# Performance work log

Hardware: AMD Instinct MI355X
Metric: run time of the kernel (lower is better)

The kernel has to match this reference:

```python
import jax, jax.numpy as jnp
import jax.scipy.linalg as jsl
import numpy as np

EPS = 1e-6          # config.eps
MIN_EIG = 1e-4      # config.min_eigenvalue
B, N, K = 2, 2048, 3


def _so3_generators():
    # standard so(3) basis: [G_c]_{kl} = -eps_{ckl}
    G = np.zeros((3, 3, 3), np.float32)
    G[0, 1, 2] = -1.0; G[0, 2, 1] = 1.0
    G[1, 0, 2] = 1.0;  G[1, 2, 0] = -1.0
    G[2, 0, 1] = -1.0; G[2, 1, 0] = 1.0
    return jnp.asarray(G)


def _spd(key, b, n, k):
    # well-conditioned SPD covariances (as a real model would produce)
    A = jax.random.normal(key, (b, n, k, k), jnp.float32)
    return jnp.einsum('bnkl,bnml->bnkm', A, A) / k + 0.5 * jnp.eye(k, dtype=jnp.float32)


def setup_inputs() -> dict:
    key = jax.random.key(0)
    k0, k1, k2, k3 = jax.random.split(key, 4)
    Sigma_prior = _spd(k0, B, N, K)
    Sigma_q = _spd(k1, B, N, K)
    phi = jax.random.normal(k2, (B, N, K), jnp.float32)          # gauge field, C == K == 3
    beta = jax.random.uniform(k3, (B, N, N), jnp.float32) / N    # attention-like weights, rows O(1)
    return {
        'Sigma_prior': Sigma_prior,
        'Sigma_q': Sigma_q,
        'phi': phi,
        'beta': beta,
        'generators': _so3_generators(),
    }


def _batched_expm(mats):
    # mats: (B, N, K, K) -> elementwise matrix exponential
    b, n, k, _ = mats.shape
    return jax.vmap(jsl.expm)(mats.reshape(-1, k, k)).reshape(b, n, k, k)


def reference(Sigma_prior, Sigma_q, phi, beta, generators):
    b, n, k, _ = Sigma_prior.shape
    I = jnp.eye(k, dtype=Sigma_prior.dtype)

    # precisions (regularized inverses)
    Lambda_p = jnp.linalg.inv(Sigma_prior + EPS * I)   # (B,N,K,K)
    Lambda_q = jnp.linalg.inv(Sigma_q + EPS * I)       # (B,N,K,K)

    # gauge transport Omega_ij = e^{phi_i} e^{-phi_j}
    phi_mat = jnp.einsum('bnc,ckl->bnkl', phi, generators)
    exp_phi = _batched_expm(phi_mat)
    exp_neg_phi = _batched_expm(-phi_mat)
    Omega = jnp.einsum('bikl,bjlm->bijkm', exp_phi, exp_neg_phi)   # (B,N,N,K,K)

    # transported neighbor precision: Omega Lambda_q Omega^T
    Lt = jnp.einsum('bijkl,bjlm,bijnm->bijkn', Omega, Lambda_q, Omega)

    # incoming social term: sum_j beta_ij * Lt_ij
    M_in = jnp.einsum('bij,bijkl->bikl', beta, Lt)

    # outgoing recoil: (sum_j beta_ji) * Lambda_q_i
    M_out = beta.sum(axis=1)[..., None, None] * Lambda_q

    M = Lambda_p + M_in + M_out
    M = 0.5 * (M + jnp.swapaxes(M, -1, -2))

    # eigenvalue floor + inverse via eigh
    w, V = jnp.linalg.eigh(M)
    w = jnp.maximum(w, MIN_EIG)
    M_pd = jnp.einsum('bnkl,bnl,bnml->bnkm', V, w, V)
    M_inv = jnp.einsum('bnkl,bnl,bnml->bnkm', V, 1.0 / w, V)
    return M_pd, M_inv
```

## Files before the change

kernel.cpp:

```cpp
#include <hip/hip_runtime.h>
#include <math.h>

#define EPS_REG 1e-6f
#define MIN_EIG_F 1e-4f
#define RB 8


__device__ __forceinline__ void sym_inv3(const float m[3][3], float o[3][3]) {
    float c00 = m[1][1]*m[2][2] - m[1][2]*m[2][1];
    float c01 = m[1][2]*m[2][0] - m[1][0]*m[2][2];
    float c02 = m[1][0]*m[2][1] - m[1][1]*m[2][0];
    float det = m[0][0]*c00 + m[0][1]*c01 + m[0][2]*c02;
    float inv = 1.0f / det;
    o[0][0] = c00*inv;
    o[1][0] = c01*inv;
    o[2][0] = c02*inv;
    o[0][1] = (m[0][2]*m[2][1]-m[0][1]*m[2][2])*inv;
    o[1][1] = (m[0][0]*m[2][2]-m[0][2]*m[2][0])*inv;
    o[2][1] = (m[0][1]*m[2][0]-m[0][0]*m[2][1])*inv;
    o[0][2] = (m[0][1]*m[1][2]-m[0][2]*m[1][1])*inv;
    o[1][2] = (m[0][2]*m[1][0]-m[0][0]*m[1][2])*inv;
    o[2][2] = (m[0][0]*m[1][1]-m[0][1]*m[1][0])*inv;
}

__device__ __forceinline__ void rodrigues(float w0, float w1, float w2, float R[3][3]) {
    float th2 = w0*w0 + w1*w1 + w2*w2;
    float th = sqrtf(th2);
    float a, b;
    if (th < 1e-4f) { a = 1.0f - th2*(1.0f/6.0f); b = 0.5f - th2*(1.0f/24.0f); }
    else            { a = sinf(th)/th;            b = (1.0f - cosf(th))/th2; }
    R[0][0] = 1.0f + b*(w0*w0 - th2); R[0][1] = -a*w2 + b*w0*w1;        R[0][2] =  a*w1 + b*w0*w2;
    R[1][0] =  a*w2 + b*w0*w1;        R[1][1] = 1.0f + b*(w1*w1 - th2); R[1][2] = -a*w0 + b*w1*w2;
    R[2][0] = -a*w1 + b*w0*w2;        R[2][1] =  a*w0 + b*w1*w2;        R[2][2] = 1.0f + b*(w2*w2 - th2);
}

__device__ __forceinline__ void jrot(float A[3][3], float V[3][3], int p, int q) {
    float apq = A[p][q];
    if (fabsf(apq) < 1e-20f) return;
    float theta = (A[q][q] - A[p][p]) / (2.0f * apq);
    float t = 1.0f / (fabsf(theta) + sqrtf(1.0f + theta*theta));
    if (theta < 0.0f) t = -t;
    float c = 1.0f / sqrtf(1.0f + t*t);
    float s = t * c;
    int r = 3 - p - q;
    float apq_t = t*apq;
    A[p][p] -= apq_t;
    A[q][q] += apq_t;
    A[p][q] = 0.0f; A[q][p] = 0.0f;
    float arp = A[r][p], arq = A[r][q];
    A[r][p] = c*arp - s*arq; A[p][r] = A[r][p];
    A[r][q] = s*arp + c*arq; A[q][r] = A[r][q];
    #pragma unroll
    for (int k = 0; k < 3; k++) {
        float vkp = V[k][p], vkq = V[k][q];
        V[k][p] = c*vkp - s*vkq;
        V[k][q] = s*vkp + c*vkq;
    }
}

__global__ __launch_bounds__(64) void precompute_S_kernel(
        const float* __restrict__ Sq,
        const float* __restrict__ phi,
        float* __restrict__ Splanes,
        int BN) {
    __shared__ float sq_s[576];
    __shared__ float ph_s[192];
    int tid = threadIdx.x;
    int p0 = blockIdx.x * 64;

    const float4* src = (const float4*)(Sq + (size_t)p0 * 9);
    #pragma unroll
    for (int i = tid; i < 144; i += 64) ((float4*)sq_s)[i] = src[i];
    const float4* psrc = (const float4*)(phi + (size_t)p0 * 3);
    if (tid < 48) ((float4*)ph_s)[tid] = psrc[tid];
    __syncthreads();

    float m[3][3], lq[3][3];
    #pragma unroll
    for (int i = 0; i < 3; i++)
        #pragma unroll
        for (int j = 0; j < 3; j++) m[i][j] = sq_s[tid*9 + i*3 + j];
    m[0][0] += EPS_REG; m[1][1] += EPS_REG; m[2][2] += EPS_REG;
    sym_inv3(m, lq);

    float R[3][3];
    rodrigues(ph_s[tid*3], ph_s[tid*3+1], ph_s[tid*3+2], R);

    float U[3][3];
    #pragma unroll
    for (int i = 0; i < 3; i++)
        #pragma unroll
        for (int j = 0; j < 3; j++)
            U[i][j] = lq[i][0]*R[0][j] + lq[i][1]*R[1][j] + lq[i][2]*R[2][j];
    float sv[6];
    sv[0] = R[0][0]*U[0][0] + R[1][0]*U[1][0] + R[2][0]*U[2][0];
    sv[1] = R[0][0]*U[0][1] + R[1][0]*U[1][1] + R[2][0]*U[2][1];
    sv[2] = R[0][0]*U[0][2] + R[1][0]*U[1][2] + R[2][0]*U[2][2];
    sv[3] = R[0][1]*U[0][1] + R[1][1]*U[1][1] + R[2][1]*U[2][1];
    sv[4] = R[0][1]*U[0][2] + R[1][1]*U[1][2] + R[2][1]*U[2][2];
    sv[5] = R[0][2]*U[0][2] + R[1][2]*U[1][2] + R[2][2]*U[2][2];
    #pragma unroll
    for (int c = 0; c < 6; c++)
        Splanes[(size_t)c * BN + p0 + tid] = sv[c];
}

__global__ __launch_bounds__(256) void fused_beta_kernel(
        const float* __restrict__ beta,
        const float* __restrict__ Splanes,
        float* __restrict__ T,
        float* __restrict__ partial,
        int B, int N, int BN) {
    int tid = threadIdx.x;
    int grow0 = blockIdx.x * RB;
    int b = grow0 / N;
    int chunksPerB = N / RB;
    int chunk = (grow0 - b * N) / RB;

    float acc[RB][6];
    #pragma unroll
    for (int r = 0; r < RB; r++)
        #pragma unroll
        for (int c = 0; c < 6; c++) acc[r][c] = 0.0f;

    int jtiles = N / 1024;
    for (int jt = 0; jt < jtiles; jt++) {
        int c0 = jt * 1024 + 4 * tid;
        float4 s[6];
        #pragma unroll
        for (int c = 0; c < 6; c++)
            s[c] = *(const float4*)(Splanes + (size_t)c * BN + (size_t)b * N + c0);

        float csum0 = 0.f, csum1 = 0.f, csum2 = 0.f, csum3 = 0.f;
        #pragma unroll
        for (int r = 0; r < RB; r++) {
            float4 w4 = *(const float4*)(beta + (size_t)(grow0 + r) * N + c0);
            csum0 += w4.x; csum1 += w4.y; csum2 += w4.z; csum3 += w4.w;
            #pragma unroll
            for (int c = 0; c < 6; c++)
                acc[r][c] += w4.x*s[c].x + w4.y*s[c].y + w4.z*s[c].z + w4.w*s[c].w;
        }
        *(float4*)(partial + ((size_t)b * chunksPerB + chunk) * N + c0) =
            make_float4(csum0, csum1, csum2, csum3);
    }

    __shared__ float red[256][48];
    __shared__ float red2[4][48];
    #pragma unroll
    for (int r = 0; r < RB; r++)
        #pragma unroll
        for (int c = 0; c < 6; c++)
            red[tid][r * 6 + c] = acc[r][c];
    __syncthreads();
    if (tid < 192) {
        int v = tid % 48, grp = tid / 48;
        float s = 0.0f;
        #pragma unroll 8
        for (int r = 0; r < 64; r++) s += red[grp * 64 + r][v];
        red2[grp][v] = s;
    }
    __syncthreads();
    if (tid < 48) {
        float v = red2[0][tid] + red2[1][tid] + red2[2][tid] + red2[3][tid];
        T[(size_t)grow0 * 6 + tid] = v;
    }
}

__global__ __launch_bounds__(256) void finalize_kernel(
        const float* __restrict__ Sp,
        const float* __restrict__ Sq,
        const float* __restrict__ phi,
        const float* __restrict__ T,
        const float* __restrict__ partial,
        float* __restrict__ out,
        int B, int N) {
    int tid   = threadIdx.x;
    int lane32 = tid & 31;
    int grp    = tid >> 5;
    int p0   = blockIdx.x * 32;
    int BN   = B * N;
    int b    = p0 / N;
    int i0   = p0 - b * N;
    int chunks = N / RB;

    __shared__ float redc[8][32];
    __shared__ float sp_s[288], sq_s[288], ph_s[96], t_s[192];
    __shared__ float o1_s[288], o2_s[288];

    int cpg = chunks / 8;
    float csp = 0.0f;
    const float* pp = partial + ((size_t)b * chunks + grp * cpg) * N + (i0 + lane32);
    #pragma unroll 8
    for (int c = 0; c < cpg; c++) { csp += *pp; pp += (size_t)N; }
    redc[grp][lane32] = csp;

    {
        const float4* s1 = (const float4*)(Sp + (size_t)p0 * 9);
        const float4* s2 = (const float4*)(Sq + (size_t)p0 * 9);
        if (tid < 72) { ((float4*)sp_s)[tid] = s1[tid]; ((float4*)sq_s)[tid] = s2[tid]; }
        const float4* s3 = (const float4*)(phi + (size_t)p0 * 3);
        if (tid < 24) ((float4*)ph_s)[tid] = s3[tid];
        const float4* s4 = (const float4*)(T + (size_t)p0 * 6);
        if (tid < 48) ((float4*)t_s)[tid] = s4[tid];
    }
    __syncthreads();

    if (tid < 32) {
        float cs = 0.0f;
        #pragma unroll
        for (int g = 0; g < 8; g++) cs += redc[g][tid];

        float m[3][3], lp[3][3], lq[3][3];
        #pragma unroll
        for (int i = 0; i < 3; i++)
            #pragma unroll
            for (int j = 0; j < 3; j++) m[i][j] = sq_s[tid*9 + i*3 + j];
        m[0][0] += EPS_REG; m[1][1] += EPS_REG; m[2][2] += EPS_REG;
        sym_inv3(m, lq);
        #pragma unroll
        for (int i = 0; i < 3; i++)
            #pragma unroll
            for (int j = 0; j < 3; j++) m[i][j] = sp_s[tid*9 + i*3 + j];
        m[0][0] += EPS_REG; m[1][1] += EPS_REG; m[2][2] += EPS_REG;
        sym_inv3(m, lp);

        float R[3][3];
        rodrigues(ph_s[tid*3], ph_s[tid*3+1], ph_s[tid*3+2], R);

        const float* tp = t_s + tid * 6;
        float Tm[3][3] = {{tp[0],tp[1],tp[2]},{tp[1],tp[3],tp[4]},{tp[2],tp[4],tp[5]}};

        float U[3][3], M[3][3];
        #pragma unroll
        for (int ii = 0; ii < 3; ii++)
            #pragma unroll
            for (int jj = 0; jj < 3; jj++)
                U[ii][jj] = R[ii][0]*Tm[0][jj] + R[ii][1]*Tm[1][jj] + R[ii][2]*Tm[2][jj];
        #pragma unroll
        for (int ii = 0; ii < 3; ii++)
            #pragma unroll
            for (int jj = 0; jj < 3; jj++) {
                float min_ij = U[ii][0]*R[jj][0] + U[ii][1]*R[jj][1] + U[ii][2]*R[jj][2];
                M[ii][jj] = lp[ii][jj] + min_ij + cs * lq[ii][jj];
            }
        float A[3][3];
        #pragma unroll
        for (int ii = 0; ii < 3; ii++)
            #pragma unroll
            for (int jj = 0; jj < 3; jj++) A[ii][jj] = 0.5f * (M[ii][jj] + M[jj][ii]);

        float V[3][3] = {{1,0,0},{0,1,0},{0,0,1}};
        #pragma unroll
        for (int sweep = 0; sweep < 6; sweep++) {
            jrot(A, V, 0, 1);
            jrot(A, V, 0, 2);
            jrot(A, V, 1, 2);
        }
        float w0 = fmaxf(A[0][0], MIN_EIG_F);
        float w1 = fmaxf(A[1][1], MIN_EIG_F);
        float w2 = fmaxf(A[2][2], MIN_EIG_F);
        float iw0 = 1.0f/w0, iw1 = 1.0f/w1, iw2 = 1.0f/w2;

        #pragma unroll
        for (int ii = 0; ii < 3; ii++)
            #pragma unroll
            for (int jj = 0; jj < 3; jj++) {
                o1_s[tid*9 + ii*3 + jj] = V[ii][0]*w0*V[jj][0] + V[ii][1]*w1*V[jj][1] + V[ii][2]*w2*V[jj][2];
                o2_s[tid*9 + ii*3 + jj] = V[ii][0]*iw0*V[jj][0] + V[ii][1]*iw1*V[jj][1] + V[ii][2]*iw2*V[jj][2];
            }
    }
    __syncthreads();

    float4* d1 = (float4*)(out + (size_t)p0 * 9);
    float4* d2 = (float4*)(out + (size_t)BN * 9 + (size_t)p0 * 9);
    if (tid < 72) { d1[tid] = ((float4*)o1_s)[tid]; d2[tid] = ((float4*)o2_s)[tid]; }
}

extern "C" void kernel_launch(void* const* d_in, const int* in_sizes, int n_in,
                              void* d_out, int out_size, void* d_ws, size_t ws_size,
                              hipStream_t stream) {
    const float* Sp   = (const float*)d_in[0];
    const float* Sq   = (const float*)d_in[1];
    const float* phi  = (const float*)d_in[2];
    const float* beta = (const float*)d_in[3];

    int BN = in_sizes[2] / 3;
    int N  = (int)((long long)in_sizes[3] / BN);
    int B  = BN / N;

    float* ws = (float*)d_ws;
    float* Splanes = ws;
    float* T       = Splanes + (size_t)BN * 6;
    float* partial = T + (size_t)BN * 6;

    float* outf = (float*)d_out;

    precompute_S_kernel<<<BN / 64, 64, 0, stream>>>(Sq, phi, Splanes, BN);

    fused_beta_kernel<<<BN / RB, 256, 0, stream>>>(beta, Splanes, T, partial, B, N, BN);

    finalize_kernel<<<BN / 32, 256, 0, stream>>>(Sp, Sq, phi, T, partial, outf, B, N);
}
```

Measured before the change: 27.31 us.

## Split beta reduction across column tiles and reduce tile partials in finalize

Result: slower. 28.98 us (+6.1%).

```diff
diff --git a/kernel.cpp b/kernel.cpp
--- a/kernel.cpp
+++ b/kernel.cpp
@@ -58,6 +58,92 @@
     }
 }
 
+__device__ __forceinline__ void compute_S_from(const float* sq9, const float* ph3, float sv[6]) {
+    float m[3][3], lq[3][3];
+    #pragma unroll
+    for (int i = 0; i < 3; i++)
+        #pragma unroll
+        for (int j = 0; j < 3; j++) m[i][j] = sq9[i*3 + j];
+    m[0][0] += EPS_REG; m[1][1] += EPS_REG; m[2][2] += EPS_REG;
+    sym_inv3(m, lq);
+    float R[3][3];
+    rodrigues(ph3[0], ph3[1], ph3[2], R);
+    float U[3][3];
+    #pragma unroll
+    for (int i = 0; i < 3; i++)
+        #pragma unroll
+        for (int j = 0; j < 3; j++)
+            U[i][j] = lq[i][0]*R[0][j] + lq[i][1]*R[1][j] + lq[i][2]*R[2][j];
+    sv[0] = R[0][0]*U[0][0] + R[1][0]*U[1][0] + R[2][0]*U[2][0];
+    sv[1] = R[0][0]*U[0][1] + R[1][0]*U[1][1] + R[2][0]*U[2][1];
+    sv[2] = R[0][0]*U[0][2] + R[1][0]*U[1][2] + R[2][0]*U[2][2];
+    sv[3] = R[0][1]*U[0][1] + R[1][1]*U[1][1] + R[2][1]*U[2][1];
+    sv[4] = R[0][1]*U[0][2] + R[1][1]*U[1][2] + R[2][1]*U[2][2];
+    sv[5] = R[0][2]*U[0][2] + R[1][2]*U[1][2] + R[2][2]*U[2][2];
+}
+
+__device__ __forceinline__ void finalize_point(const float* sq9, const float* sp9,
+                                               const float* ph3, const float* tp,
+                                               float cs, float* o1, float* o2) {
+    float m[3][3], lp[3][3], lq[3][3];
+    #pragma unroll
+    for (int i = 0; i < 3; i++)
+        #pragma unroll
+        for (int j = 0; j < 3; j++) m[i][j] = sq9[i*3 + j];
+    m[0][0] += EPS_REG; m[1][1] += EPS_REG; m[2][2] += EPS_REG;
+    sym_inv3(m, lq);
+    #pragma unroll
+    for (int i = 0; i < 3; i++)
+        #pragma unroll
+        for (int j = 0; j < 3; j++) m[i][j] = sp9[i*3 + j];
+    m[0][0] += EPS_REG; m[1][1] += EPS_REG; m[2][2] += EPS_REG;
+    sym_inv3(m, lp);
+
+    float R[3][3];
+    rodrigues(ph3[0], ph3[1], ph3[2], R);
+
+    float Tm[3][3] = {{tp[0],tp[1],tp[2]},{tp[1],tp[3],tp[4]},{tp[2],tp[4],tp[5]}};
+
+    float U[3][3], M[3][3];
+    #pragma unroll
+    for (int ii = 0; ii < 3; ii++)
+        #pragma unroll
+        for (int jj = 0; jj < 3; jj++)
+            U[ii][jj] = R[ii][0]*Tm[0][jj] + R[ii][1]*Tm[1][jj] + R[ii][2]*Tm[2][jj];
+    #pragma unroll
+    for (int ii = 0; ii < 3; ii++)
+        #pragma unroll
+        for (int jj = 0; jj < 3; jj++) {
+            float min_ij = U[ii][0]*R[jj][0] + U[ii][1]*R[jj][1] + U[ii][2]*R[jj][2];
+            M[ii][jj] = lp[ii][jj] + min_ij + cs * lq[ii][jj];
+        }
+    float A[3][3];
+    #pragma unroll
+    for (int ii = 0; ii < 3; ii++)
+        #pragma unroll
+        for (int jj = 0; jj < 3; jj++) A[ii][jj] = 0.5f * (M[ii][jj] + M[jj][ii]);
+
+    float V[3][3] = {{1,0,0},{0,1,0},{0,0,1}};
+    #pragma unroll
+    for (int sweep = 0; sweep < 6; sweep++) {
+        jrot(A, V, 0, 1);
+        jrot(A, V, 0, 2);
+        jrot(A, V, 1, 2);
+    }
+    float w0 = fmaxf(A[0][0], MIN_EIG_F);
+    float w1 = fmaxf(A[1][1], MIN_EIG_F);
+    float w2 = fmaxf(A[2][2], MIN_EIG_F);
+    float iw0 = 1.0f/w0, iw1 = 1.0f/w1, iw2 = 1.0f/w2;
+
+    #pragma unroll
+    for (int ii = 0; ii < 3; ii++)
+        #pragma unroll
+        for (int jj = 0; jj < 3; jj++) {
+            o1[ii*3 + jj] = V[ii][0]*w0*V[jj][0] + V[ii][1]*w1*V[jj][1] + V[ii][2]*w2*V[jj][2];
+            o2[ii*3 + jj] = V[ii][0]*iw0*V[jj][0] + V[ii][1]*iw1*V[jj][1] + V[ii][2]*iw2*V[jj][2];
+        }
+}
+
 __global__ __launch_bounds__(64) void precompute_S_kernel(
         const float* __restrict__ Sq,
         const float* __restrict__ phi,
@@ -75,93 +161,81 @@
     if (tid < 48) ((float4*)ph_s)[tid] = psrc[tid];
     __syncthreads();
 
-    float m[3][3], lq[3][3];
-    #pragma unroll
-    for (int i = 0; i < 3; i++)
-        #pragma unroll
-        for (int j = 0; j < 3; j++) m[i][j] = sq_s[tid*9 + i*3 + j];
-    m[0][0] += EPS_REG; m[1][1] += EPS_REG; m[2][2] += EPS_REG;
-    sym_inv3(m, lq);
-
-    float R[3][3];
-    rodrigues(ph_s[tid*3], ph_s[tid*3+1], ph_s[tid*3+2], R);
-
-    float U[3][3];
-    #pragma unroll
-    for (int i = 0; i < 3; i++)
-        #pragma unroll
-        for (int j = 0; j < 3; j++)
-            U[i][j] = lq[i][0]*R[0][j] + lq[i][1]*R[1][j] + lq[i][2]*R[2][j];
     float sv[6];
-    sv[0] = R[0][0]*U[0][0] + R[1][0]*U[1][0] + R[2][0]*U[2][0];
-    sv[1] = R[0][0]*U[0][1] + R[1][0]*U[1][1] + R[2][0]*U[2][1];
-    sv[2] = R[0][0]*U[0][2] + R[1][0]*U[1][2] + R[2][0]*U[2][2];
-    sv[3] = R[0][1]*U[0][1] + R[1][1]*U[1][1] + R[2][1]*U[2][1];
-    sv[4] = R[0][1]*U[0][2] + R[1][1]*U[1][2] + R[2][1]*U[2][2];
-    sv[5] = R[0][2]*U[0][2] + R[1][2]*U[1][2] + R[2][2]*U[2][2];
+    compute_S_from(sq_s + tid*9, ph_s + tid*3, sv);
     #pragma unroll
     for (int c = 0; c < 6; c++)
         Splanes[(size_t)c * BN + p0 + tid] = sv[c];
 }
 
-__global__ __launch_bounds__(256) void fused_beta_kernel(
+__global__ __launch_bounds__(256, 4) void fused_beta_kernel(
         const float* __restrict__ beta,
         const float* __restrict__ Splanes,
-        float* __restrict__ T,
+        float* __restrict__ T2,
         float* __restrict__ partial,
         int B, int N, int BN) {
     int tid = threadIdx.x;
-    int grow0 = blockIdx.x * RB;
+    int ctiles = N >> 10;
+    int rg = blockIdx.x / ctiles;
+    int ct = blockIdx.x - rg * ctiles;
+    int grow0 = rg * RB;
     int b = grow0 / N;
     int chunksPerB = N / RB;
     int chunk = (grow0 - b * N) / RB;
+    int c0 = (ct << 10) + 4 * tid;
+
+    float4 s[6], w[RB];
+    #pragma unroll
+    for (int c = 0; c < 6; c++)
+        s[c] = *(const float4*)(Splanes + (size_t)c * BN + (size_t)b * N + c0);
+    #pragma unroll
+    for (int r = 0; r < RB; r++)
+        w[r] = *(const float4*)(beta + (size_t)(grow0 + r) * N + c0);
+
+    float csum0 = 0.f, csum1 = 0.f, csum2 = 0.f, csum3 = 0.f;
+    #pragma unroll
+    for (int r = 0; r < RB; r++) {
+        csum0 += w[r].x; csum1 += w[r].y; csum2 += w[r].z; csum3 += w[r].w;
+    }
+    *(float4*)(partial + ((size_t)b * chunksPerB + chunk) * N + c0) =
+        make_float4(csum0, csum1, csum2, csum3);
 
     float acc[RB][6];
     #pragma unroll
     for (int r = 0; r < RB; r++)
         #pragma unroll
-        for (int c = 0; c < 6; c++) acc[r][c] = 0.0f;
-
-    int jtiles = N / 1024;
-    for (int jt = 0; jt < jtiles; jt++) {
-        int c0 = jt * 1024 + 4 * tid;
-        float4 s[6];
-        #pragma unroll
         for (int c = 0; c < 6; c++)
-            s[c] = *(const float4*)(Splanes + (size_t)c * BN + (size_t)b * N + c0);
-
-        float csum0 = 0.f, csum1 = 0.f, csum2 = 0.f, csum3 = 0.f;
-        #pragma unroll
-        for (int r = 0; r < RB; r++) {
-            float4 w4 = *(const float4*)(beta + (size_t)(grow0 + r) * N + c0);
-            csum0 += w4.x; csum1 += w4.y; csum2 += w4.z; csum3 += w4.w;
+            acc[r][c] = w[r].x*s[c].x + w[r].y*s[c].y + w[r].z*s[c].z + w[r].w*s[c].w;
+
+    __shared__ float red[128][48];
+    __shared__ float red2[4][48];
+    if (tid < 128) {
+        #pragma unroll
+        for (int r = 0; r < RB; r++)
             #pragma unroll
             for (int c = 0; c < 6; c++)
-                acc[r][c] += w4.x*s[c].x + w4.y*s[c].y + w4.z*s[c].z + w4.w*s[c].w;
-        }
-        *(float4*)(partial + ((size_t)b * chunksPerB + chunk) * N + c0) =
-            make_float4(csum0, csum1, csum2, csum3);
-    }
-
-    __shared__ float red[256][48];
-    __shared__ float red2[4][48];
-    #pragma unroll
-    for (int r = 0; r < RB; r++)
-        #pragma unroll
-        for (int c = 0; c < 6; c++)
-            red[tid][r * 6 + c] = acc[r][c];
+                red[tid][r * 6 + c] = acc[r][c];
+    }
+    __syncthreads();
+    if (tid >= 128) {
+        #pragma unroll
+        for (int r = 0; r < RB; r++)
+            #pragma unroll
+            for (int c = 0; c < 6; c++)
+                red[tid - 128][r * 6 + c] += acc[r][c];
+    }
     __syncthreads();
     if (tid < 192) {
         int v = tid % 48, grp = tid / 48;
-        float s = 0.0f;
+        float sum = 0.0f;
         #pragma unroll 8
-        for (int r = 0; r < 64; r++) s += red[grp * 64 + r][v];
-        red2[grp][v] = s;
+        for (int r = 0; r < 32; r++) sum += red[grp * 32 + r][v];
+        red2[grp][v] = sum;
     }
     __syncthreads();
     if (tid < 48) {
         float v = red2[0][tid] + red2[1][tid] + red2[2][tid] + red2[3][tid];
-        T[(size_t)grow0 * 6 + tid] = v;
+        T2[((size_t)ct * BN + grow0) * 6 + tid] = v;
     }
 }
 
@@ -169,104 +243,61 @@
         const float* __restrict__ Sp,
         const float* __restrict__ Sq,
         const float* __restrict__ phi,
-        const float* __restrict__ T,
+        const float* __restrict__ T2,
         const float* __restrict__ partial,
         float* __restrict__ out,
         int B, int N) {
-    int tid   = threadIdx.x;
-    int lane32 = tid & 31;
-    int grp    = tid >> 5;
+    int tid  = threadIdx.x;
     int p0   = blockIdx.x * 32;
     int BN   = B * N;
     int b    = p0 / N;
     int i0   = p0 - b * N;
     int chunks = N / RB;
-
-    __shared__ float redc[8][32];
+    int ctiles = N >> 10;
+
+    __shared__ float4 redc[32][8];
     __shared__ float sp_s[288], sq_s[288], ph_s[96], t_s[192];
     __shared__ float o1_s[288], o2_s[288];
 
-    int cpg = chunks / 8;
-    float csp = 0.0f;
-    const float* pp = partial + ((size_t)b * chunks + grp * cpg) * N + (i0 + lane32);
-    #pragma unroll 8
-    for (int c = 0; c < cpg; c++) { csp += *pp; pp += (size_t)N; }
-    redc[grp][lane32] = csp;
-
+    {
+        int m = tid & 7;
+        int g = tid >> 3;
+        int cpg = chunks / 32;
+        float4 a = make_float4(0.f, 0.f, 0.f, 0.f);
+        const float4* pp = (const float4*)(partial + ((size_t)b * chunks + g * cpg) * N + i0) + m;
+        int stepq = N >> 2;
+        for (int k = 0; k < cpg; k++) {
+            float4 v = *pp; pp += stepq;
+            a.x += v.x; a.y += v.y; a.z += v.z; a.w += v.w;
+        }
+        redc[g][m] = a;
+    }
     {
         const float4* s1 = (const float4*)(Sp + (size_t)p0 * 9);
         const float4* s2 = (const float4*)(Sq + (size_t)p0 * 9);
         if (tid < 72) { ((float4*)sp_s)[tid] = s1[tid]; ((float4*)sq_s)[tid] = s2[tid]; }
         const float4* s3 = (const float4*)(phi + (size_t)p0 * 3);
         if (tid < 24) ((float4*)ph_s)[tid] = s3[tid];
-        const float4* s4 = (const float4*)(T + (size_t)p0 * 6);
-        if (tid < 48) ((float4*)t_s)[tid] = s4[tid];
+        if (tid < 48) {
+            float4 a = make_float4(0.f, 0.f, 0.f, 0.f);
+            for (int ct = 0; ct < ctiles; ct++) {
+                float4 v = ((const float4*)(T2 + ((size_t)ct * BN + p0) * 6))[tid];
+                a.x += v.x; a.y += v.y; a.z += v.z; a.w += v.w;
+            }
+            ((float4*)t_s)[tid] = a;
+        }
     }
     __syncthreads();
 
     if (tid < 32) {
         float cs = 0.0f;
         #pragma unroll
-        for (int g = 0; g < 8; g++) cs += redc[g][tid];
-
-        float m[3][3], lp[3][3], lq[3][3];
-        #pragma unroll
-        for (int i = 0; i < 3; i++)
-            #pragma unroll
-            for (int j = 0; j < 3; j++) m[i][j] = sq_s[tid*9 + i*3 + j];
-        m[0][0] += EPS_REG; m[1][1] += EPS_REG; m[2][2] += EPS_REG;
-        sym_inv3(m, lq);
-        #pragma unroll
-        for (int i = 0; i < 3; i++)
-            #pragma unroll
-            for (int j = 0; j < 3; j++) m[i][j] = sp_s[tid*9 + i*3 + j];
-        m[0][0] += EPS_REG; m[1][1] += EPS_REG; m[2][2] += EPS_REG;
-        sym_inv3(m, lp);
-
-        float R[3][3];
-        rodrigues(ph_s[tid*3], ph_s[tid*3+1], ph_s[tid*3+2], R);
-
-        const float* tp = t_s + tid * 6;
-        float Tm[3][3] = {{tp[0],tp[1],tp[2]},{tp[1],tp[3],tp[4]},{tp[2],tp[4],tp[5]}};
-
-        float U[3][3], M[3][3];
-        #pragma unroll
-        for (int ii = 0; ii < 3; ii++)
-            #pragma unroll
-            for (int jj = 0; jj < 3; jj++)
-                U[ii][jj] = R[ii][0]*Tm[0][jj] + R[ii][1]*Tm[1][jj] + R[ii][2]*Tm[2][jj];
-        #pragma unroll
-        for (int ii = 0; ii < 3; ii++)
-            #pragma unroll
-            for (int jj = 0; jj < 3; jj++) {
-                float min_ij = U[ii][0]*R[jj][0] + U[ii][1]*R[jj][1] + U[ii][2]*R[jj][2];
-                M[ii][jj] = lp[ii][jj] + min_ij + cs * lq[ii][jj];
-            }
-        float A[3][3];
-        #pragma unroll
-        for (int ii = 0; ii < 3; ii++)
-            #pragma unroll
-            for (int jj = 0; jj < 3; jj++) A[ii][jj] = 0.5f * (M[ii][jj] + M[jj][ii]);
-
-        float V[3][3] = {{1,0,0},{0,1,0},{0,0,1}};
-        #pragma unroll
-        for (int sweep = 0; sweep < 6; sweep++) {
-            jrot(A, V, 0, 1);
-            jrot(A, V, 0, 2);
-            jrot(A, V, 1, 2);
-        }
-        float w0 = fmaxf(A[0][0], MIN_EIG_F);
-        float w1 = fmaxf(A[1][1], MIN_EIG_F);
-        float w2 = fmaxf(A[2][2], MIN_EIG_F);
-        float iw0 = 1.0f/w0, iw1 = 1.0f/w1, iw2 = 1.0f/w2;
-
-        #pragma unroll
-        for (int ii = 0; ii < 3; ii++)
-            #pragma unroll
-            for (int jj = 0; jj < 3; jj++) {
-                o1_s[tid*9 + ii*3 + jj] = V[ii][0]*w0*V[jj][0] + V[ii][1]*w1*V[jj][1] + V[ii][2]*w2*V[jj][2];
-                o2_s[tid*9 + ii*3 + jj] = V[ii][0]*iw0*V[jj][0] + V[ii][1]*iw1*V[jj][1] + V[ii][2]*iw2*V[jj][2];
-            }
+        for (int g = 0; g < 32; g++) {
+            const float* rc = (const float*)&redc[g][tid >> 2];
+            cs += rc[tid & 3];
+        }
+        finalize_point(sq_s + tid*9, sp_s + tid*9, ph_s + tid*3,
+                       t_s + tid*6, cs, o1_s + tid*9, o2_s + tid*9);
     }
     __syncthreads();
 
@@ -286,17 +317,19 @@
     int BN = in_sizes[2] / 3;
     int N  = (int)((long long)in_sizes[3] / BN);
     int B  = BN / N;
+    int ctiles = N >> 10;
 
     float* ws = (float*)d_ws;
     float* Splanes = ws;
-    float* T       = Splanes + (size_t)BN * 6;
-    float* partial = T + (size_t)BN * 6;
+    float* T2      = Splanes + (size_t)BN * 6;
+    float* partial = T2 + (size_t)ctiles * BN * 6;
 
     float* outf = (float*)d_out;
 
     precompute_S_kernel<<<BN / 64, 64, 0, stream>>>(Sq, phi, Splanes, BN);
 
-    fused_beta_kernel<<<BN / RB, 256, 0, stream>>>(beta, Splanes, T, partial, B, N, BN);
-
-    finalize_kernel<<<BN / 32, 256, 0, stream>>>(Sp, Sq, phi, T, partial, outf, B, N);
-}
+    fused_beta_kernel<<<(BN / RB) * ctiles, 256, 0, stream>>>(
+        beta, Splanes, T2, partial, B, N, BN);
+
+    finalize_kernel<<<BN / 32, 256, 0, stream>>>(Sp, Sq, phi, T2, partial, outf, B, N);
+}
```
